# Kernel optimization log

Measured on AMD Instinct MI355X. Metric: run time of the kernel, lower is better.

The kernel has to match this reference:

```python
import jax, jax.numpy as jnp
import numpy as np

B, C, D, H, W = 2, 64, 16, 16, 16
C8 = C // 8

def setup_inputs() -> dict:
    key = jax.random.key(0)
    ks = jax.random.split(key, 8)
    x = jax.random.normal(ks[0], (B, C, D, H, W), dtype=jnp.float32)
    # 1x1x1 Conv3d == pointwise linear over channels
    Wq = jax.random.normal(ks[1], (C8, C), dtype=jnp.float32) * 0.05
    bq = jax.random.normal(ks[2], (C8,), dtype=jnp.float32) * 0.02
    Wk = jax.random.normal(ks[3], (C8, C), dtype=jnp.float32) * 0.05
    bk = jax.random.normal(ks[4], (C8,), dtype=jnp.float32) * 0.02
    Wv = jax.random.normal(ks[5], (C, C), dtype=jnp.float32) * 0.05
    bv = jax.random.normal(ks[6], (C,), dtype=jnp.float32) * 0.02
    # original inits gamma=0 (identity output); use nonzero so attention path is exercised
    gamma = jnp.asarray([0.5], dtype=jnp.float32)
    return {"x": x, "Wq": Wq, "bq": bq, "Wk": Wk, "bk": bk, "Wv": Wv, "bv": bv, "gamma": gamma}

def reference(x, Wq, bq, Wk, bk, Wv, bv, gamma):
    b, c, d, h, w = x.shape
    n = d * h * w
    xf = x.reshape(b, c, n)                                   # (B, C, N)
    q = jnp.einsum('oc,bcn->bon', Wq, xf) + bq[None, :, None]  # (B, C8, N)
    k = jnp.einsum('oc,bcn->bon', Wk, xf) + bk[None, :, None]  # (B, C8, N)
    v = jnp.einsum('oc,bcn->bon', Wv, xf) + bv[None, :, None]  # (B, C,  N)
    energy = jnp.einsum('bci,bcj->bij', q, k)                  # (B, N, N) = Q^T K
    attn = jax.nn.softmax(energy, axis=-1)
    out = jnp.einsum('bcj,bij->bci', v, attn)                  # V @ attn^T
    out = out.reshape(b, c, d, h, w)
    return gamma[0] * out + x
```

## Files before the change

### kernel.cpp

```cpp
#include <hip/hip_runtime.h>
#include <hip/hip_bf16.h>

typedef __hip_bfloat16 bf16;
typedef __attribute__((ext_vector_type(8))) short short8;
typedef __attribute__((ext_vector_type(4))) float float4v;
typedef __attribute__((ext_vector_type(4))) unsigned int uint4v;

static constexpr int NN = 4096;
static constexpr int CC = 64;
static constexpr int BB = 2;
static constexpr int WV = 16;

template <typename T> __device__ __forceinline__ float cvt_in(T v);
template <> __device__ __forceinline__ float cvt_in<float>(float v) { return v; }
template <> __device__ __forceinline__ float cvt_in<bf16>(bf16 v) { return __bfloat162float(v); }

__device__ __forceinline__ unsigned int f2b(float f) {
    return (unsigned int)__builtin_bit_cast(unsigned short, __float2bfloat16(f));
}

__device__ __forceinline__ int block_detect_bf16(const void* x, float* sred) {
    const bf16* xb = (const bf16*)x;
    float mx = 0.f;
    for (int t = threadIdx.x; t < 1024; t += blockDim.x) {
        float a = fabsf(__bfloat162float(xb[t]));
        if (!(a < 1e30f)) a = 1e30f;
        mx = fmaxf(mx, a);
    }
#pragma unroll
    for (int off = 32; off; off >>= 1) mx = fmaxf(mx, __shfl_xor(mx, off));
    const int nw = blockDim.x >> 6;
    if ((threadIdx.x & 63) == 0) sred[threadIdx.x >> 6] = mx;
    __syncthreads();
    float m = 0.f;
    for (int wv = 0; wv < nw; ++wv) m = fmaxf(m, sred[wv]);
    return m < 1000.f ? 1 : 0;
}

template <typename TIO>
__device__ __forceinline__ void proj_body(
    const TIO* __restrict__ x,
    const TIO* __restrict__ Wq, const TIO* __restrict__ bq,
    const TIO* __restrict__ Wk, const TIO* __restrict__ bk,
    const TIO* __restrict__ Wv, const TIO* __restrict__ bv,
    unsigned short* __restrict__ qT, unsigned short* __restrict__ kT,
    unsigned short* __restrict__ vfrag, float* sW, float* sb, float* part)
{
    const int tid  = threadIdx.x;
    const int colq = tid & 63;
    const int cq   = tid >> 6;
    const int col  = blockIdx.x * 64 + colq;
    const int b    = col >> 12;
    const int n    = col & (NN - 1);
    const int og   = blockIdx.y;

    if (og == 0) {
        for (int t = tid; t < 1024; t += 256) {
            int r = t >> 6, c = t & 63;
            sW[t] = cvt_in<TIO>(r < 8 ? Wq[r * 64 + c] : Wk[(r - 8) * 64 + c]);
        }
        if (tid < 16)
            sb[tid] = cvt_in<TIO>(tid < 8 ? bq[tid] : bk[tid - 8]);
    } else {
        const int r0 = (og - 1) * 16;
        for (int t = tid; t < 1024; t += 256)
            sW[t] = cvt_in<TIO>(Wv[(r0 + (t >> 6)) * 64 + (t & 63)]);
        if (tid < 16)
            sb[tid] = cvt_in<TIO>(bv[r0 + tid]);
    }
    __syncthreads();

    float xv[16];
    const TIO* xb = x + ((size_t)b * CC + cq * 16) * NN + n;
#pragma unroll
    for (int c = 0; c < 16; ++c) xv[c] = cvt_in<TIO>(xb[(size_t)c * NN]);

    float acc[16];
#pragma unroll
    for (int o = 0; o < 16; ++o) {
        float a = 0.f;
#pragma unroll
        for (int c = 0; c < 16; ++c)
            a = fmaf(sW[o * 64 + cq * 16 + c], xv[c], a);
        acc[o] = a;
    }

    if (cq > 0) {
#pragma unroll
        for (int o = 0; o < 16; ++o)
            part[((cq - 1) * 16 + o) * 64 + colq] = acc[o];
    }
    __syncthreads();
    if (cq != 0) return;

#pragma unroll
    for (int o = 0; o < 16; ++o)
        acc[o] += sb[o] + part[o * 64 + colq] + part[(16 + o) * 64 + colq] +
                  part[(32 + o) * 64 + colq];

    if (og == 0) {
        unsigned short row[16];
#pragma unroll
        for (int o = 0; o < 16; ++o) row[o] = (unsigned short)f2b(acc[o]);
        *(short8*)(qT + (size_t)(b * NN + n) * 8) = *(const short8*)&row[0];
        *(short8*)(kT + (size_t)(b * NN + n) * 8) = *(const short8*)&row[8];
    } else {
        unsigned short* vt = vfrag +
            (size_t)((b * 128 + (n >> 5)) * 4 + (og - 1)) * 512 +
            ((n >> 3) & 3) * 128 + (n & 7);
#pragma unroll
        for (int o = 0; o < 16; ++o)
            vt[o * 8] = (unsigned short)f2b(acc[o]);
    }
}

__global__ __launch_bounds__(256) void proj_kernel(
    const void* x, const void* Wq, const void* bq, const void* Wk,
    const void* bk, const void* Wv, const void* bv,
    unsigned short* qT, unsigned short* kT, unsigned short* vfrag)
{
    __shared__ float sW[16 * 64];
    __shared__ float sb[16];
    __shared__ float part[3 * 16 * 64];
    __shared__ float sred[4];
    const int bf = block_detect_bf16(x, sred);
    __syncthreads();
    if (bf)
        proj_body<bf16>((const bf16*)x, (const bf16*)Wq, (const bf16*)bq,
                        (const bf16*)Wk, (const bf16*)bk, (const bf16*)Wv,
                        (const bf16*)bv, qT, kT, vfrag, sW, sb, part);
    else
        proj_body<float>((const float*)x, (const float*)Wq, (const float*)bq,
                         (const float*)Wk, (const float*)bk, (const float*)Wv,
                         (const float*)bv, qT, kT, vfrag, sW, sb, part);
}

struct AttnUnit {
    short8 kf[2];
    short8 vf[4];
};

__device__ __forceinline__ void load_unit(
    const unsigned short* __restrict__ kTb,
    const unsigned short* __restrict__ vfb,
    int j0, int quad, int m, int lane, AttnUnit& U)
{
    const short8 zero8 = {};
#pragma unroll
    for (int js = 0; js < 2; ++js) {
        U.kf[js] = zero8;
        if (quad == 0)
            U.kf[js] = *(const short8*)(kTb + (size_t)(j0 + js * 16 + m) * 8);
    }
    const int jblk = j0 >> 5;
#pragma unroll
    for (int cs = 0; cs < 4; ++cs)
        U.vf[cs] = *(const short8*)(
            vfb + (size_t)(jblk * 4 + cs) * 512 + lane * 8);
}

__device__ __forceinline__ void compute_unit(
    const AttnUnit& U, const short8& qf, int srcA, int srcB, bool hi,
    float4v acc[4], float& lsum)
{
    const float4v zero4 = {0.f, 0.f, 0.f, 0.f};
    unsigned int p0[2], p1[2];
#pragma unroll
    for (int js = 0; js < 2; ++js) {
        const float4v st =
            __builtin_amdgcn_mfma_f32_16x16x32_bf16(U.kf[js], qf, zero4, 0, 0, 0);
        float e0 = __expf(st[0]), e1 = __expf(st[1]);
        float e2 = __expf(st[2]), e3 = __expf(st[3]);
        lsum += (e0 + e1) + (e2 + e3);
        p0[js] = f2b(e0) | (f2b(e1) << 16);
        p1[js] = f2b(e2) | (f2b(e3) << 16);
    }
    const unsigned int A0a = __shfl((int)p0[0], srcA);
    const unsigned int A1a = __shfl((int)p1[0], srcA);
    const unsigned int B0a = __shfl((int)p0[0], srcB);
    const unsigned int B1a = __shfl((int)p1[0], srcB);
    const unsigned int A0b = __shfl((int)p0[1], srcA);
    const unsigned int A1b = __shfl((int)p1[1], srcA);
    const unsigned int B0b = __shfl((int)p0[1], srcB);
    const unsigned int B1b = __shfl((int)p1[1], srcB);
    uint4v pw;
    pw.x = hi ? A0b : A0a;
    pw.y = hi ? A1b : A1a;
    pw.z = hi ? B0b : B0a;
    pw.w = hi ? B1b : B1a;
    const short8 pb = __builtin_bit_cast(short8, pw);
#pragma unroll
    for (int cs = 0; cs < 4; ++cs)
        acc[cs] = __builtin_amdgcn_mfma_f32_16x16x32_bf16(
            U.vf[cs], pb, acc[cs], 0, 0, 0);
}

__global__ __launch_bounds__(1024, 4) void attn_kernel(
    const unsigned short* __restrict__ qT, const unsigned short* __restrict__ kT,
    const unsigned short* __restrict__ vfrag,
    const void* __restrict__ xv, const void* __restrict__ gammav, void* outv)
{
    __shared__ float redpool[WV * 1024];
    __shared__ float lpart[WV][16];
    __shared__ float sred[WV];

    const int bf = block_detect_bf16(xv, sred);

    const int w    = threadIdx.x >> 6;
    const int lane = threadIdx.x & 63;
    const int m    = lane & 15;
    const int quad = lane >> 4;
    const int b    = blockIdx.x >> 8;
    const int i0   = (blockIdx.x & 255) << 4;

    const short8  zero8 = {};
    const float4v zero4 = {0.f, 0.f, 0.f, 0.f};

    short8 qf = zero8;
    if (quad == 0)
        qf = *(const short8*)(qT + (size_t)(b * NN + i0 + m) * 8);

    float4v acc[4] = {zero4, zero4, zero4, zero4};
    float lsum = 0.f;

    const unsigned short* kTb = kT + (size_t)b * NN * 8;
    const unsigned short* vfb = vfrag + (size_t)b * 128 * 4 * 512;

    const int srcA = 32 * (quad & 1) + m;
    const int srcB = srcA + 16;
    const bool hi  = (quad >> 1) != 0;

    const int jbase = w * (NN / WV);

    AttnUnit A, B;
    load_unit(kTb, vfb, jbase, quad, m, lane, A);
#pragma unroll
    for (int u = 0; u < 8; u += 2) {
        load_unit(kTb, vfb, jbase + (u + 1) * 32, quad, m, lane, B);
        compute_unit(A, qf, srcA, srcB, hi, acc, lsum);
        if (u + 2 < 8)
            load_unit(kTb, vfb, jbase + (u + 2) * 32, quad, m, lane, A);
        compute_unit(B, qf, srcA, srcB, hi, acc, lsum);
    }

    lsum += __shfl_xor(lsum, 16);
    lsum += __shfl_xor(lsum, 32);
    if (lane < 16) lpart[w][lane] = lsum;

    float* redw = redpool + w * 1024;
#pragma unroll
    for (int cs = 0; cs < 4; ++cs)
#pragma unroll
        for (int r = 0; r < 4; ++r)
            redw[(cs * 4 + r) * 64 + lane] = acc[cs][r];
    __syncthreads();

    float lt = 0.f;
#pragma unroll
    for (int wv = 0; wv < WV; ++wv) lt += lpart[wv][m];
    const float linv = 1.f / lt;

    float v = 0.f;
#pragma unroll
    for (int wv = 0; wv < WV; ++wv) v += redpool[wv * 1024 + w * 64 + lane];

    const int c  = (w >> 2) * 16 + quad * 4 + (w & 3);
    const int ig = i0 + m;
    const size_t off = ((size_t)b * CC + c) * NN + ig;

    if (bf) {
        const float gl = __bfloat162float(((const bf16*)gammav)[0]) * linv;
        ((bf16*)outv)[off] = __float2bfloat16(
            fmaf(gl, v, __bfloat162float(((const bf16*)xv)[off])));
    } else {
        const float gl = ((const float*)gammav)[0] * linv;
        ((float*)outv)[off] = fmaf(gl, v, ((const float*)xv)[off]);
    }
}

extern "C" void kernel_launch(void* const* d_in, const int* in_sizes, int n_in,
                              void* d_out, int out_size, void* d_ws, size_t ws_size,
                              hipStream_t stream)
{
    const void* x     = d_in[0];
    const void* Wq    = d_in[1];
    const void* bq    = d_in[2];
    const void* Wk    = d_in[3];
    const void* bk    = d_in[4];
    const void* Wv    = d_in[5];
    const void* bv    = d_in[6];
    const void* gamma = d_in[7];

    unsigned short* qT    = (unsigned short*)d_ws;
    unsigned short* kT    = qT + (size_t)BB * NN * 8;
    unsigned short* vfrag = kT + (size_t)BB * NN * 8;

    proj_kernel<<<dim3(BB * NN / 64, 5), 256, 0, stream>>>(
        x, Wq, bq, Wk, bk, Wv, bv, qT, kT, vfrag);
    attn_kernel<<<BB * (NN / 16), 1024, 0, stream>>>(
        qT, kT, vfrag, x, gamma, d_out);
}
```

Before: 95.93 us.

## Permute K rows so MFMA score output feeds PV MFMA without shuffles

Each lane now loads K rows in a permuted order (jperm), so the QK^T MFMA result already sits in the lane/k layout the second MFMA expects for its B operand. That removes the eight cross-lane shuffles and selects per 32-key unit. The explicit A/B double-buffered load/compute structs are replaced by a simple loop with unroll 2 and interleaved V loads. The launch-bounds occupancy hint is raised from 4 to 8, which may tighten the register budget and risks spills.

```diff
diff --git a/kernel.cpp b/kernel.cpp
--- a/kernel.cpp
+++ b/kernel.cpp
@@ -135,67 +135,7 @@
                          (const float*)bv, qT, kT, vfrag, sW, sb, part);
 }
 
-struct AttnUnit {
-    short8 kf[2];
-    short8 vf[4];
-};
-
-__device__ __forceinline__ void load_unit(
-    const unsigned short* __restrict__ kTb,
-    const unsigned short* __restrict__ vfb,
-    int j0, int quad, int m, int lane, AttnUnit& U)
-{
-    const short8 zero8 = {};
-#pragma unroll
-    for (int js = 0; js < 2; ++js) {
-        U.kf[js] = zero8;
-        if (quad == 0)
-            U.kf[js] = *(const short8*)(kTb + (size_t)(j0 + js * 16 + m) * 8);
-    }
-    const int jblk = j0 >> 5;
-#pragma unroll
-    for (int cs = 0; cs < 4; ++cs)
-        U.vf[cs] = *(const short8*)(
-            vfb + (size_t)(jblk * 4 + cs) * 512 + lane * 8);
-}
-
-__device__ __forceinline__ void compute_unit(
-    const AttnUnit& U, const short8& qf, int srcA, int srcB, bool hi,
-    float4v acc[4], float& lsum)
-{
-    const float4v zero4 = {0.f, 0.f, 0.f, 0.f};
-    unsigned int p0[2], p1[2];
-#pragma unroll
-    for (int js = 0; js < 2; ++js) {
-        const float4v st =
-            __builtin_amdgcn_mfma_f32_16x16x32_bf16(U.kf[js], qf, zero4, 0, 0, 0);
-        float e0 = __expf(st[0]), e1 = __expf(st[1]);
-        float e2 = __expf(st[2]), e3 = __expf(st[3]);
-        lsum += (e0 + e1) + (e2 + e3);
-        p0[js] = f2b(e0) | (f2b(e1) << 16);
-        p1[js] = f2b(e2) | (f2b(e3) << 16);
-    }
-    const unsigned int A0a = __shfl((int)p0[0], srcA);
-    const unsigned int A1a = __shfl((int)p1[0], srcA);
-    const unsigned int B0a = __shfl((int)p0[0], srcB);
-    const unsigned int B1a = __shfl((int)p1[0], srcB);
-    const unsigned int A0b = __shfl((int)p0[1], srcA);
-    const unsigned int A1b = __shfl((int)p1[1], srcA);
-    const unsigned int B0b = __shfl((int)p0[1], srcB);
-    const unsigned int B1b = __shfl((int)p1[1], srcB);
-    uint4v pw;
-    pw.x = hi ? A0b : A0a;
-    pw.y = hi ? A1b : A1a;
-    pw.z = hi ? B0b : B0a;
-    pw.w = hi ? B1b : B1a;
-    const short8 pb = __builtin_bit_cast(short8, pw);
-#pragma unroll
-    for (int cs = 0; cs < 4; ++cs)
-        acc[cs] = __builtin_amdgcn_mfma_f32_16x16x32_bf16(
-            U.vf[cs], pb, acc[cs], 0, 0, 0);
-}
-
-__global__ __launch_bounds__(1024, 4) void attn_kernel(
+__global__ __launch_bounds__(1024, 8) void attn_kernel(
     const unsigned short* __restrict__ qT, const unsigned short* __restrict__ kT,
     const unsigned short* __restrict__ vfrag,
     const void* __restrict__ xv, const void* __restrict__ gammav, void* outv)
@@ -226,21 +166,47 @@
     const unsigned short* kTb = kT + (size_t)b * NN * 8;
     const unsigned short* vfb = vfrag + (size_t)b * 128 * 4 * 512;
 
-    const int srcA = 32 * (quad & 1) + m;
-    const int srcB = srcA + 16;
-    const bool hi  = (quad >> 1) != 0;
-
+    const int jperm = ((m >> 2) << 3) + (m & 3);
     const int jbase = w * (NN / WV);
 
-    AttnUnit A, B;
-    load_unit(kTb, vfb, jbase, quad, m, lane, A);
-#pragma unroll
-    for (int u = 0; u < 8; u += 2) {
-        load_unit(kTb, vfb, jbase + (u + 1) * 32, quad, m, lane, B);
-        compute_unit(A, qf, srcA, srcB, hi, acc, lsum);
-        if (u + 2 < 8)
-            load_unit(kTb, vfb, jbase + (u + 2) * 32, quad, m, lane, A);
-        compute_unit(B, qf, srcA, srcB, hi, acc, lsum);
+#pragma unroll 2
+    for (int u = 0; u < 8; ++u) {
+        const int j0 = jbase + u * 32;
+
+        short8 kf1 = zero8, kf2 = zero8;
+        if (quad == 0) {
+            const unsigned short* kp = kTb + (size_t)(j0 + jperm) * 8;
+            kf1 = *(const short8*)kp;
+            kf2 = *(const short8*)(kp + 32);
+        }
+        const unsigned short* vt = vfb + (size_t)(j0 >> 5) * 4 * 512 + lane * 8;
+        const short8 vf0 = *(const short8*)(vt);
+        const short8 vf1 = *(const short8*)(vt + 512);
+
+        const float4v st1 =
+            __builtin_amdgcn_mfma_f32_16x16x32_bf16(kf1, qf, zero4, 0, 0, 0);
+        const float4v st2 =
+            __builtin_amdgcn_mfma_f32_16x16x32_bf16(kf2, qf, zero4, 0, 0, 0);
+
+        const float e0 = __expf(st1[0]), e1 = __expf(st1[1]);
+        const float e2 = __expf(st1[2]), e3 = __expf(st1[3]);
+        const float f0 = __expf(st2[0]), f1 = __expf(st2[1]);
+        const float f2 = __expf(st2[2]), f3 = __expf(st2[3]);
+        lsum += ((e0 + e1) + (e2 + e3)) + ((f0 + f1) + (f2 + f3));
+
+        uint4v pw;
+        pw.x = f2b(e0) | (f2b(e1) << 16);
+        pw.y = f2b(e2) | (f2b(e3) << 16);
+        pw.z = f2b(f0) | (f2b(f1) << 16);
+        pw.w = f2b(f2) | (f2b(f3) << 16);
+        const short8 pb = __builtin_bit_cast(short8, pw);
+
+        acc[0] = __builtin_amdgcn_mfma_f32_16x16x32_bf16(vf0, pb, acc[0], 0, 0, 0);
+        const short8 vf2 = *(const short8*)(vt + 1024);
+        acc[1] = __builtin_amdgcn_mfma_f32_16x16x32_bf16(vf1, pb, acc[1], 0, 0, 0);
+        const short8 vf3 = *(const short8*)(vt + 1536);
+        acc[2] = __builtin_amdgcn_mfma_f32_16x16x32_bf16(vf2, pb, acc[2], 0, 0, 0);
+        acc[3] = __builtin_amdgcn_mfma_f32_16x16x32_bf16(vf3, pb, acc[3], 0, 0, 0);
     }
 
     lsum += __shfl_xor(lsum, 16);
```

Result: no change. 94.61 us (-1.4%).
